# Kernel optimization log

Hardware: AMD Instinct MI355X
Metric: run time of the kernel (lower is better)

Reference implementation:

```python
import jax, jax.numpy as jnp
import numpy as np

B, S, D, H = 2, 2048, 1024, 16
DK = D // H


def setup_inputs() -> dict:
    key = jax.random.key(0)
    ks = jax.random.split(key, 14)
    inp = {
        'query': jax.random.normal(ks[0], (B, S, D), jnp.float32),
        'key': jax.random.normal(ks[1], (B, S, D), jnp.float32),
        'value': jax.random.normal(ks[2], (B, S, D), jnp.float32),
        'mask': jax.random.randint(ks[3], (B, 1, S, S), 0, 2).astype(bool),
        'rel_pos_bias': jax.random.normal(ks[4], (1, H, S, S), jnp.float32),
    }
    scale = 1.0 / np.sqrt(D)
    names = ['Wq', 'bq', 'Wk', 'bk', 'Wv', 'bv', 'Wo', 'bo']
    for i, n in enumerate(names):
        k = ks[5 + i]
        if n.startswith('W'):
            inp[n] = jax.random.normal(k, (D, D), jnp.float32) * scale
        else:
            inp[n] = jnp.zeros((D,), jnp.float32)
    return inp


def reference(query, key, value, mask, rel_pos_bias, Wq, bq, Wk, bk, Wv, bv, Wo, bo):
    # torch Linear: y = x @ W^T + b; W stored [out, in]
    def proj(x, W, b):
        y = x @ W.T + b                       # [B,S,D]
        return y.reshape(B, S, H, DK).transpose(0, 2, 1, 3)  # [B,H,S,DK]

    q = proj(query, Wq, bq)
    k = proj(key, Wk, bk)
    v = proj(value, Wv, bv)

    scores = jnp.einsum('bhqd,bhkd->bhqk', q, k) / jnp.sqrt(jnp.float32(DK))
    scores = scores + rel_pos_bias
    scores = jnp.where(mask, jnp.float32(-1e9), scores)
    p_attn = jax.nn.softmax(scores, axis=-1)
    x = jnp.einsum('bhqk,bhkd->bhqd', p_attn, v)  # [B,H,S,DK]
    x = x.transpose(0, 2, 1, 3).reshape(B, S, D)
    return x @ Wo.T + bo
```

## Files before the change

kernel.cpp:

```cpp
#include <hip/hip_runtime.h>
#include <stdint.h>


typedef _Float16 f16;
typedef _Float16 f16x8 __attribute__((ext_vector_type(8)));
typedef _Float16 f16x4 __attribute__((ext_vector_type(4)));
typedef float f32x4 __attribute__((ext_vector_type(4)));

#define LOG2E 1.44269504088896340736f

__device__ __forceinline__ void gload16(const void* g, void* l) {
  __builtin_amdgcn_global_load_lds(
      (const __attribute__((address_space(1))) unsigned int*)g,
      (__attribute__((address_space(3))) unsigned int*)l, 16, 0, 0);
}

__global__ __launch_bounds__(256) void cvt_f32_f16(const float* __restrict__ in,
                                                   f16* __restrict__ out, int n4) {
  const int i = blockIdx.x * 256 + threadIdx.x;
  if (i >= n4) return;
  const float4 v = ((const float4*)in)[i];
  f16x4 o = {(f16)v.x, (f16)v.y, (f16)v.z, (f16)v.w};
  ((f16x4*)out)[i] = o;
}

__global__ void mask_detect(const uint8_t* __restrict__ m, int* __restrict__ flag) {
  __shared__ int s_off, s_weird;
  const int t = threadIdx.x;
  if (t == 0) { s_off = 0; s_weird = 0; }
  __syncthreads();
  int f_off = 0, f_weird = 0;
  for (int i = t; i < 8192; i += 256) {
    const uint8_t v = m[i];
    if ((i & 3) && v) f_off = 1;
    if (v > 1) f_weird = 1;
  }
  if (f_off) atomicOr(&s_off, 1);
  if (f_weird) atomicOr(&s_weird, 1);
  __syncthreads();
  if (t == 0) *flag = (s_off && !s_weird) ? 1 : 0;
}

__global__ __launch_bounds__(256) void mask_canon(const uint8_t* __restrict__ m,
                                                  uint8_t* __restrict__ out,
                                                  const int* __restrict__ flag) {
  const int i = (blockIdx.x * 256 + threadIdx.x) * 4;
  uchar4 o;
  if (*flag) {
    const uchar4 v = *(const uchar4*)(m + i);
    o = make_uchar4(v.x != 0, v.y != 0, v.z != 0, v.w != 0);
  } else {
    const int4 v = *(const int4*)((const int*)m + i);
    o = make_uchar4(v.x != 0, v.y != 0, v.z != 0, v.w != 0);
  }
  *(uchar4*)(out + i) = o;
}

template <int MODE>
__global__ __launch_bounds__(256, 2) void gemm_bt(const f16* __restrict__ A,
                                                  const f16* __restrict__ Bw,
                                                  const float* __restrict__ bias,
                                                  void* __restrict__ outp) {
  constexpr int K = 1024;
  const int t = threadIdx.x;
  const int w = t >> 6, lane = t & 63, l15 = lane & 15, l4 = lane >> 4;
  const int bm = (int)(blockIdx.x >> 4) * 128;
  const int bn = (int)(blockIdx.x & 15) * 64;

  __shared__ f16 As[2][128 * 32];
  __shared__ f16 Bs[2][64 * 32];

  const f16* a0 = A + (size_t)(bm + (t >> 2)) * K + (t & 3) * 8;
  const f16* a1 = a0 + (size_t)64 * K;
  const f16* b0 = Bw + (size_t)(bn + (t >> 2)) * K + (t & 3) * 8;

  f32x4 acc[2][4];
#pragma unroll
  for (int m = 0; m < 2; ++m)
#pragma unroll
    for (int n = 0; n < 4; ++n) acc[m][n] = (f32x4){0.f, 0.f, 0.f, 0.f};

#define STAGE_G(buf, k0)                          \
  do {                                            \
    gload16(a0 + (k0), &As[buf][w * 512]);        \
    gload16(a1 + (k0), &As[buf][2048 + w * 512]); \
    gload16(b0 + (k0), &Bs[buf][w * 512]);        \
  } while (0)

  STAGE_G(0, 0);
  __syncthreads();
  int cur = 0;
#pragma unroll 1
  for (int kt = 0; kt < 32; ++kt) {
    if (kt < 31) STAGE_G(cur ^ 1, (kt + 1) * 32);
    const f16* ap = &As[cur][(w * 32 + l15) * 32 + l4 * 8];
    const f16* bp = &Bs[cur][l15 * 32 + l4 * 8];
    f16x8 af[2], bfr[4];
#pragma unroll
    for (int m = 0; m < 2; ++m) af[m] = *(const f16x8*)(ap + m * 512);
#pragma unroll
    for (int n = 0; n < 4; ++n) bfr[n] = *(const f16x8*)(bp + n * 512);
#pragma unroll
    for (int m = 0; m < 2; ++m)
#pragma unroll
      for (int n = 0; n < 4; ++n)
        acc[m][n] = __builtin_amdgcn_mfma_f32_16x16x32_f16(af[m], bfr[n], acc[m][n], 0, 0, 0);
    __syncthreads();
    cur ^= 1;
  }
#undef STAGE_G

#pragma unroll
  for (int m = 0; m < 2; ++m) {
    const int r0 = bm + w * 32 + m * 16 + (l4 << 2);
#pragma unroll
    for (int n = 0; n < 4; ++n) {
      const int c = bn + n * 16 + l15;
      const float bv = bias[c];
#pragma unroll
      for (int j = 0; j < 4; ++j) {
        const int r = r0 + j;
        const float v = acc[m][n][j] + bv;
        if (MODE == 0) {
          const int b_ = r >> 11, s = r & 2047, h_ = c >> 6, dk = c & 63;
          ((f16*)outp)[(((size_t)b_ * 16 + h_) * 2048 + s) * 64 + dk] = (f16)v;
        } else if (MODE == 1) {
          const int b_ = r >> 11, s = r & 2047, h_ = c >> 6, dk = c & 63;
          ((f16*)outp)[(((size_t)b_ * 16 + h_) * 64 + dk) * 2048 + s] = (f16)v;
        } else {
          ((float*)outp)[(size_t)r * 1024 + c] = v;
        }
      }
    }
  }
}

__device__ __forceinline__ const f16x8* swzr(const f16* base, int row, int bytecol) {
  return (const f16x8*)((const char*)base + row * 128 + (bytecol ^ ((row & 7) << 4)));
}

__global__ __launch_bounds__(256, 4) void attn_fwd(
    const f16* __restrict__ Qp, const f16* __restrict__ Kp,
    const f16* __restrict__ Vt, const float* __restrict__ bias,
    const uint8_t* __restrict__ mask, f16* __restrict__ X) {
  constexpr int S = 2048;
  const int bid = blockIdx.x;
  const int qt = bid & 31, b = (bid >> 5) & 1, h = bid >> 6;
  const int t = threadIdx.x, w = t >> 6, lane = t & 63;
  const int l15 = lane & 15, l4 = lane >> 4;
  const int q0 = qt * 64 + w * 16;

  const f16* Qbh = Qp + (size_t)(b * 16 + h) * S * 64;
  const f16* Kbh = Kp + (size_t)(b * 16 + h) * S * 64;
  const f16* Vbh = Vt + (size_t)(b * 16 + h) * 64 * S;
  const float* biash = bias + (size_t)h * S * S;
  const uint8_t* maskb = mask + (size_t)b * S * S;

  __shared__ f16 Ks[64 * 64];
  __shared__ f16 Vs[64 * 64];
  __shared__ f16 Ps[4][16 * 64];

  int ro[4];
#pragma unroll
  for (int j = 0; j < 4; ++j) ro[j] = (q0 + l4 * 4 + j) * S + l15;

  f16x8 qf[2];
#pragma unroll
  for (int ks = 0; ks < 2; ++ks)
    qf[ks] = *(const f16x8*)(Qbh + (size_t)(q0 + l15) * 64 + ks * 32 + l4 * 8);

  f32x4 oacc[4];
#pragma unroll
  for (int n = 0; n < 4; ++n) oacc[n] = (f32x4){0.f, 0.f, 0.f, 0.f};
  float mrow[4], lrow[4];
#pragma unroll
  for (int j = 0; j < 4; ++j) { mrow[j] = -3e38f; lrow[j] = 0.f; }

  const int srow = t >> 3;
  const int scol = (((t & 7) ^ (srow & 7)) << 3);

#pragma unroll 1
  for (int kt = 0; kt < 32; ++kt) {
    const int k0 = kt * 64;
    __syncthreads();
    gload16(Kbh + (size_t)(k0 + srow) * 64 + scol, &Ks[w * 512]);
    gload16(Kbh + (size_t)(k0 + 32 + srow) * 64 + scol, &Ks[2048 + w * 512]);
    gload16(Vbh + (size_t)srow * S + k0 + scol, &Vs[w * 512]);
    gload16(Vbh + (size_t)(32 + srow) * S + k0 + scol, &Vs[2048 + w * 512]);
    float breg[4][4];
    int mreg[4][4];
#pragma unroll
    for (int j = 0; j < 4; ++j)
#pragma unroll
      for (int n = 0; n < 4; ++n) {
        breg[j][n] = biash[ro[j] + k0 + n * 16];
        mreg[j][n] = maskb[ro[j] + k0 + n * 16];
      }
    __syncthreads();

    f32x4 sacc[4];
#pragma unroll
    for (int n = 0; n < 4; ++n) sacc[n] = (f32x4){0.f, 0.f, 0.f, 0.f};
#pragma unroll
    for (int n = 0; n < 4; ++n)
#pragma unroll
      for (int ks = 0; ks < 2; ++ks) {
        const f16x8 kf = *swzr(Ks, n * 16 + l15, ks * 64 + l4 * 16);
        sacc[n] = __builtin_amdgcn_mfma_f32_16x16x32_f16(qf[ks], kf, sacc[n], 0, 0, 0);
      }

    float p[4][4];
    float tmax[4];
#pragma unroll
    for (int j = 0; j < 4; ++j) tmax[j] = -3e38f;
#pragma unroll
    for (int j = 0; j < 4; ++j)
#pragma unroll
      for (int n = 0; n < 4; ++n) {
        float s = sacc[n][j] * 0.125f + breg[j][n];
        s = mreg[j][n] ? -1e9f : s;
        p[j][n] = s;
        tmax[j] = fmaxf(tmax[j], s);
      }
#pragma unroll
    for (int j = 0; j < 4; ++j) {
      float v = tmax[j];
      v = fmaxf(v, __shfl_xor(v, 1));
      v = fmaxf(v, __shfl_xor(v, 2));
      v = fmaxf(v, __shfl_xor(v, 4));
      v = fmaxf(v, __shfl_xor(v, 8));
      tmax[j] = v;
    }

#pragma unroll
    for (int j = 0; j < 4; ++j) {
      const float mnew = fmaxf(mrow[j], tmax[j]);
      const float alpha = __builtin_exp2f((mrow[j] - mnew) * LOG2E);
      mrow[j] = mnew;
      lrow[j] *= alpha;
#pragma unroll
      for (int n = 0; n < 4; ++n) oacc[n][j] *= alpha;
      float lsum = 0.f;
      const int prow = l4 * 4 + j;
#pragma unroll
      for (int n = 0; n < 4; ++n) {
        const float e = __builtin_exp2f((p[j][n] - mnew) * LOG2E);
        lsum += e;
        const int bc = (n * 16 + l15) * 2;
        *(f16*)((char*)&Ps[w][0] + prow * 128 + (bc ^ ((prow & 7) << 4))) = (f16)e;
      }
      lsum += __shfl_xor(lsum, 1);
      lsum += __shfl_xor(lsum, 2);
      lsum += __shfl_xor(lsum, 4);
      lsum += __shfl_xor(lsum, 8);
      lrow[j] += lsum;
    }

    f16x8 pf[2];
#pragma unroll
    for (int ks = 0; ks < 2; ++ks)
      pf[ks] = *swzr(&Ps[w][0], l15, ks * 64 + l4 * 16);
#pragma unroll
    for (int ks = 0; ks < 2; ++ks)
#pragma unroll
      for (int n = 0; n < 4; ++n) {
        const f16x8 vf = *swzr(Vs, n * 16 + l15, ks * 64 + l4 * 16);
        oacc[n] = __builtin_amdgcn_mfma_f32_16x16x32_f16(pf[ks], vf, oacc[n], 0, 0, 0);
      }
  }

#pragma unroll
  for (int j = 0; j < 4; ++j) {
    const float inv = 1.0f / lrow[j];
    const int qrow = q0 + l4 * 4 + j;
#pragma unroll
    for (int n = 0; n < 4; ++n) {
      const int dk = n * 16 + l15;
      X[((size_t)b * 2048 + qrow) * 1024 + h * 64 + dk] = (f16)(oacc[n][j] * inv);
    }
  }
}

extern "C" void kernel_launch(void* const* d_in, const int* in_sizes, int n_in,
                              void* d_out, int out_size, void* d_ws, size_t ws_size,
                              hipStream_t stream) {
  const float* query = (const float*)d_in[0];
  const float* key_ = (const float*)d_in[1];
  const float* value = (const float*)d_in[2];
  const uint8_t* mask = (const uint8_t*)d_in[3];
  const float* bias = (const float*)d_in[4];
  const float* Wq = (const float*)d_in[5];
  const float* bq = (const float*)d_in[6];
  const float* Wk = (const float*)d_in[7];
  const float* bk = (const float*)d_in[8];
  const float* Wv = (const float*)d_in[9];
  const float* bv = (const float*)d_in[10];
  const float* Wo = (const float*)d_in[11];
  const float* bo = (const float*)d_in[12];

  char* p = (char*)d_ws;
  f16* qh = (f16*)p; p += (size_t)4194304 * 2;
  f16* kh = (f16*)p; p += (size_t)4194304 * 2;
  f16* vh = (f16*)p; p += (size_t)4194304 * 2;
  f16* wqh = (f16*)p; p += (size_t)1048576 * 2;
  f16* wkh = (f16*)p; p += (size_t)1048576 * 2;
  f16* wvh = (f16*)p; p += (size_t)1048576 * 2;
  f16* woh = (f16*)p; p += (size_t)1048576 * 2;
  f16* Qp = (f16*)p; p += (size_t)4194304 * 2;
  f16* Kp = (f16*)p; p += (size_t)4194304 * 2;
  f16* Vt = (f16*)p; p += (size_t)4194304 * 2;
  f16* Xh = (f16*)p; p += (size_t)4194304 * 2;
  uint8_t* m8 = (uint8_t*)p; p += (size_t)8388608;
  int* flag = (int*)p; p += 256;
  if (ws_size < (size_t)(p - (char*)d_ws)) return;

  mask_detect<<<1, 256, 0, stream>>>(mask, flag);
  mask_canon<<<8192, 256, 0, stream>>>(mask, m8, flag);

  cvt_f32_f16<<<4096, 256, 0, stream>>>(query, qh, 1048576);
  cvt_f32_f16<<<4096, 256, 0, stream>>>(key_, kh, 1048576);
  cvt_f32_f16<<<4096, 256, 0, stream>>>(value, vh, 1048576);
  cvt_f32_f16<<<1024, 256, 0, stream>>>(Wq, wqh, 262144);
  cvt_f32_f16<<<1024, 256, 0, stream>>>(Wk, wkh, 262144);
  cvt_f32_f16<<<1024, 256, 0, stream>>>(Wv, wvh, 262144);
  cvt_f32_f16<<<1024, 256, 0, stream>>>(Wo, woh, 262144);

  gemm_bt<0><<<512, 256, 0, stream>>>(qh, wqh, bq, Qp);
  gemm_bt<0><<<512, 256, 0, stream>>>(kh, wkh, bk, Kp);
  gemm_bt<1><<<512, 256, 0, stream>>>(vh, wvh, bv, Vt);

  attn_fwd<<<1024, 256, 0, stream>>>(Qp, Kp, Vt, bias, m8, Xh);

  gemm_bt<2><<<512, 256, 0, stream>>>(Xh, woh, bo, d_out);
}
```

Before: 299.6 us.

## Double-buffer K/V tiles, transpose score MFMA, fold softmax scale into Q projection

The attention kernel now double-buffers the K/V shared-memory tiles and prefetches the next tile's bias and mask into registers, so global loads overlap the current tile's compute and one barrier per iteration is dropped. The QK MFMA operands are swapped so each lane holds a single query row. That allows vectorized f32x4 bias and 32-bit mask loads, reductions with only two cross-lane shuffles, and packed f16x4 stores of P. The 1/sqrt(dk)*log2e factor is folded into the Q projection epilogue, which removes per-element scaling in the inner loop. Costs are double the K/V LDS, extra registers for prefetched data, and Q stored in f16 with the log2e scale applied.

```diff
diff --git a/kernel.cpp b/kernel.cpp
--- a/kernel.cpp
+++ b/kernel.cpp
@@ -60,7 +60,8 @@
 __global__ __launch_bounds__(256, 2) void gemm_bt(const f16* __restrict__ A,
                                                   const f16* __restrict__ Bw,
                                                   const float* __restrict__ bias,
-                                                  void* __restrict__ outp) {
+                                                  void* __restrict__ outp,
+                                                  float scale) {
   constexpr int K = 1024;
   const int t = threadIdx.x;
   const int w = t >> 6, lane = t & 63, l15 = lane & 15, l4 = lane >> 4;
@@ -120,7 +121,7 @@
 #pragma unroll
       for (int j = 0; j < 4; ++j) {
         const int r = r0 + j;
-        const float v = acc[m][n][j] + bv;
+        const float v = (acc[m][n][j] + bv) * scale;
         if (MODE == 0) {
           const int b_ = r >> 11, s = r & 2047, h_ = c >> 6, dk = c & 63;
           ((f16*)outp)[(((size_t)b_ * 16 + h_) * 2048 + s) * 64 + dk] = (f16)v;
@@ -153,16 +154,12 @@
   const f16* Qbh = Qp + (size_t)(b * 16 + h) * S * 64;
   const f16* Kbh = Kp + (size_t)(b * 16 + h) * S * 64;
   const f16* Vbh = Vt + (size_t)(b * 16 + h) * 64 * S;
-  const float* biash = bias + (size_t)h * S * S;
-  const uint8_t* maskb = mask + (size_t)b * S * S;
-
-  __shared__ f16 Ks[64 * 64];
-  __shared__ f16 Vs[64 * 64];
+  const float* biasr = bias + (size_t)h * S * S + (size_t)(q0 + l15) * S + l4 * 4;
+  const uint8_t* maskr = mask + (size_t)b * S * S + (size_t)(q0 + l15) * S + l4 * 4;
+
+  __shared__ f16 Ks[2][64 * 64];
+  __shared__ f16 Vs[2][64 * 64];
   __shared__ f16 Ps[4][16 * 64];
-
-  int ro[4];
-#pragma unroll
-  for (int j = 0; j < 4; ++j) ro[j] = (q0 + l4 * 4 + j) * S + l15;
 
   f16x8 qf[2];
 #pragma unroll
@@ -172,112 +169,130 @@
   f32x4 oacc[4];
 #pragma unroll
   for (int n = 0; n < 4; ++n) oacc[n] = (f32x4){0.f, 0.f, 0.f, 0.f};
-  float mrow[4], lrow[4];
-#pragma unroll
-  for (int j = 0; j < 4; ++j) { mrow[j] = -3e38f; lrow[j] = 0.f; }
+  float mrow = -3e38f, lrow = 0.f;
 
   const int srow = t >> 3;
   const int scol = (((t & 7) ^ (srow & 7)) << 3);
 
+#define STAGE(bf, kk)                                                              \
+  do {                                                                             \
+    gload16(Kbh + (size_t)((kk) + srow) * 64 + scol, &Ks[bf][w * 512]);            \
+    gload16(Kbh + (size_t)((kk) + 32 + srow) * 64 + scol, &Ks[bf][2048 + w * 512]);\
+    gload16(Vbh + (size_t)srow * S + (kk) + scol, &Vs[bf][w * 512]);               \
+    gload16(Vbh + (size_t)(32 + srow) * S + (kk) + scol, &Vs[bf][2048 + w * 512]); \
+  } while (0)
+
+  STAGE(0, 0);
+  f32x4 bcur[4];
+  uint32_t mcur[4];
+#pragma unroll
+  for (int n = 0; n < 4; ++n) {
+    bcur[n] = *(const f32x4*)(biasr + n * 16);
+    mcur[n] = *(const uint32_t*)(maskr + n * 16);
+  }
+  __syncthreads();
+
+  int buf = 0;
 #pragma unroll 1
   for (int kt = 0; kt < 32; ++kt) {
     const int k0 = kt * 64;
+    f32x4 bnxt[4];
+    uint32_t mnxt[4];
+    if (kt < 31) {
+      STAGE(buf ^ 1, k0 + 64);
+#pragma unroll
+      for (int n = 0; n < 4; ++n) {
+        bnxt[n] = *(const f32x4*)(biasr + k0 + 64 + n * 16);
+        mnxt[n] = *(const uint32_t*)(maskr + k0 + 64 + n * 16);
+      }
+    }
+
+    f32x4 sacc[4];
+#pragma unroll
+    for (int n = 0; n < 4; ++n) sacc[n] = (f32x4){0.f, 0.f, 0.f, 0.f};
+#pragma unroll
+    for (int n = 0; n < 4; ++n)
+#pragma unroll
+      for (int ks = 0; ks < 2; ++ks) {
+        const f16x8 kf = *swzr(&Ks[buf][0], n * 16 + l15, ks * 64 + l4 * 16);
+        sacc[n] = __builtin_amdgcn_mfma_f32_16x16x32_f16(kf, qf[ks], sacc[n], 0, 0, 0);
+      }
+
+    float tmax = -3e38f;
+#pragma unroll
+    for (int n = 0; n < 4; ++n)
+#pragma unroll
+      for (int j = 0; j < 4; ++j) {
+        float s = fmaf(bcur[n][j], LOG2E, sacc[n][j]);
+        s = ((mcur[n] >> (8 * j)) & 255u) ? -1.44269504e9f : s;
+        sacc[n][j] = s;
+        tmax = fmaxf(tmax, s);
+      }
+    tmax = fmaxf(tmax, __shfl_xor(tmax, 16));
+    tmax = fmaxf(tmax, __shfl_xor(tmax, 32));
+
+    const float mnew = fmaxf(mrow, tmax);
+    const float alpha = __builtin_exp2f(mrow - mnew);
+    mrow = mnew;
+    float lsum = 0.f;
+#pragma unroll
+    for (int n = 0; n < 4; ++n)
+#pragma unroll
+      for (int j = 0; j < 4; ++j) {
+        const float e = __builtin_exp2f(sacc[n][j] - mnew);
+        sacc[n][j] = e;
+        lsum += e;
+      }
+    lsum += __shfl_xor(lsum, 16);
+    lsum += __shfl_xor(lsum, 32);
+    lrow = lrow * alpha + lsum;
+
+    float aq[4];
+#pragma unroll
+    for (int j = 0; j < 4; ++j) aq[j] = __shfl(alpha, l4 * 4 + j);
+#pragma unroll
+    for (int n = 0; n < 4; ++n)
+#pragma unroll
+      for (int j = 0; j < 4; ++j) oacc[n][j] *= aq[j];
+
+#pragma unroll
+    for (int n = 0; n < 4; ++n) {
+      f16x4 pk = {(f16)sacc[n][0], (f16)sacc[n][1], (f16)sacc[n][2], (f16)sacc[n][3]};
+      *(f16x4*)((char*)&Ps[w][0] + l15 * 128 +
+                ((32 * n + 8 * l4) ^ ((l15 & 7) << 4))) = pk;
+    }
+
+    f16x8 pf[2];
+#pragma unroll
+    for (int ks = 0; ks < 2; ++ks) pf[ks] = *swzr(&Ps[w][0], l15, ks * 64 + l4 * 16);
+#pragma unroll
+    for (int ks = 0; ks < 2; ++ks)
+#pragma unroll
+      for (int n = 0; n < 4; ++n) {
+        const f16x8 vf = *swzr(&Vs[buf][0], n * 16 + l15, ks * 64 + l4 * 16);
+        oacc[n] = __builtin_amdgcn_mfma_f32_16x16x32_f16(pf[ks], vf, oacc[n], 0, 0, 0);
+      }
+
     __syncthreads();
-    gload16(Kbh + (size_t)(k0 + srow) * 64 + scol, &Ks[w * 512]);
-    gload16(Kbh + (size_t)(k0 + 32 + srow) * 64 + scol, &Ks[2048 + w * 512]);
-    gload16(Vbh + (size_t)srow * S + k0 + scol, &Vs[w * 512]);
-    gload16(Vbh + (size_t)(32 + srow) * S + k0 + scol, &Vs[2048 + w * 512]);
-    float breg[4][4];
-    int mreg[4][4];
-#pragma unroll
-    for (int j = 0; j < 4; ++j)
-#pragma unroll
-      for (int n = 0; n < 4; ++n) {
-        breg[j][n] = biash[ro[j] + k0 + n * 16];
-        mreg[j][n] = maskb[ro[j] + k0 + n * 16];
-      }
-    __syncthreads();
-
-    f32x4 sacc[4];
-#pragma unroll
-    for (int n = 0; n < 4; ++n) sacc[n] = (f32x4){0.f, 0.f, 0.f, 0.f};
-#pragma unroll
-    for (int n = 0; n < 4; ++n)
-#pragma unroll
-      for (int ks = 0; ks < 2; ++ks) {
-        const f16x8 kf = *swzr(Ks, n * 16 + l15, ks * 64 + l4 * 16);
-        sacc[n] = __builtin_amdgcn_mfma_f32_16x16x32_f16(qf[ks], kf, sacc[n], 0, 0, 0);
-      }
-
-    float p[4][4];
-    float tmax[4];
-#pragma unroll
-    for (int j = 0; j < 4; ++j) tmax[j] = -3e38f;
-#pragma unroll
-    for (int j = 0; j < 4; ++j)
-#pragma unroll
-      for (int n = 0; n < 4; ++n) {
-        float s = sacc[n][j] * 0.125f + breg[j][n];
-        s = mreg[j][n] ? -1e9f : s;
-        p[j][n] = s;
-        tmax[j] = fmaxf(tmax[j], s);
-      }
-#pragma unroll
-    for (int j = 0; j < 4; ++j) {
-      float v = tmax[j];
-      v = fmaxf(v, __shfl_xor(v, 1));
-      v = fmaxf(v, __shfl_xor(v, 2));
-      v = fmaxf(v, __shfl_xor(v, 4));
-      v = fmaxf(v, __shfl_xor(v, 8));
-      tmax[j] = v;
+    buf ^= 1;
+    if (kt < 31) {
+#pragma unroll
+      for (int n = 0; n < 4; ++n) { bcur[n] = bnxt[n]; mcur[n] = mnxt[n]; }
     }
-
-#pragma unroll
-    for (int j = 0; j < 4; ++j) {
-      const float mnew = fmaxf(mrow[j], tmax[j]);
-      const float alpha = __builtin_exp2f((mrow[j] - mnew) * LOG2E);
-      mrow[j] = mnew;
-      lrow[j] *= alpha;
-#pragma unroll
-      for (int n = 0; n < 4; ++n) oacc[n][j] *= alpha;
-      float lsum = 0.f;
-      const int prow = l4 * 4 + j;
-#pragma unroll
-      for (int n = 0; n < 4; ++n) {
-        const float e = __builtin_exp2f((p[j][n] - mnew) * LOG2E);
-        lsum += e;
-        const int bc = (n * 16 + l15) * 2;
-        *(f16*)((char*)&Ps[w][0] + prow * 128 + (bc ^ ((prow & 7) << 4))) = (f16)e;
-      }
-      lsum += __shfl_xor(lsum, 1);
-      lsum += __shfl_xor(lsum, 2);
-      lsum += __shfl_xor(lsum, 4);
-      lsum += __shfl_xor(lsum, 8);
-      lrow[j] += lsum;
-    }
-
-    f16x8 pf[2];
-#pragma unroll
-    for (int ks = 0; ks < 2; ++ks)
-      pf[ks] = *swzr(&Ps[w][0], l15, ks * 64 + l4 * 16);
-#pragma unroll
-    for (int ks = 0; ks < 2; ++ks)
-#pragma unroll
-      for (int n = 0; n < 4; ++n) {
-        const f16x8 vf = *swzr(Vs, n * 16 + l15, ks * 64 + l4 * 16);
-        oacc[n] = __builtin_amdgcn_mfma_f32_16x16x32_f16(pf[ks], vf, oacc[n], 0, 0, 0);
-      }
-  }
-
+  }
+#undef STAGE
+
+  const float inv = 1.0f / lrow;
+  float invq[4];
+#pragma unroll
+  for (int j = 0; j < 4; ++j) invq[j] = __shfl(inv, l4 * 4 + j);
 #pragma unroll
   for (int j = 0; j < 4; ++j) {
-    const float inv = 1.0f / lrow[j];
     const int qrow = q0 + l4 * 4 + j;
 #pragma unroll
-    for (int n = 0; n < 4; ++n) {
-      const int dk = n * 16 + l15;
-      X[((size_t)b * 2048 + qrow) * 1024 + h * 64 + dk] = (f16)(oacc[n][j] * inv);
-    }
+    for (int n = 0; n < 4; ++n)
+      X[((size_t)b * 2048 + qrow) * 1024 + h * 64 + n * 16 + l15] =
+          (f16)(oacc[n][j] * invq[j]);
   }
 }
 
@@ -325,11 +340,11 @@
   cvt_f32_f16<<<1024, 256, 0, stream>>>(Wv, wvh, 262144);
   cvt_f32_f16<<<1024, 256, 0, stream>>>(Wo, woh, 262144);
 
-  gemm_bt<0><<<512, 256, 0, stream>>>(qh, wqh, bq, Qp);
-  gemm_bt<0><<<512, 256, 0, stream>>>(kh, wkh, bk, Kp);
-  gemm_bt<1><<<512, 256, 0, stream>>>(vh, wvh, bv, Vt);
+  gemm_bt<0><<<512, 256, 0, stream>>>(qh, wqh, bq, Qp, 0.125f * LOG2E);
+  gemm_bt<0><<<512, 256, 0, stream>>>(kh, wkh, bk, Kp, 1.0f);
+  gemm_bt<1><<<512, 256, 0, stream>>>(vh, wvh, bv, Vt, 1.0f);
 
   attn_fwd<<<1024, 256, 0, stream>>>(Qp, Kp, Vt, bias, m8, Xh);
 
-  gemm_bt<2><<<512, 256, 0, stream>>>(Xh, woh, bo, d_out);
-}
+  gemm_bt<2><<<512, 256, 0, stream>>>(Xh, woh, bo, d_out, 1.0f);
+}
```

Measured after the change: 310.8 us. +3.8%, slower.
